# Performance work log

Measured on AMD Instinct MI355X. Metric: run time of the kernel, lower is better.

The kernel has to match this reference:

```python
import jax, jax.numpy as jnp
import numpy as np
import math

R0, R1 = 0.5, 40.0            # radius_range
SP0, SP1 = 8, 8               # social_pooling_size
HID = 48                      # hidden_size
INP = 96                      # input_size (32 img feat + 16 vel + 48 fsp)
N_OTHERS = 400000
RADIUS_STEP = (R1 - R0) / SP0
THETA_STEP = 2.0 * math.pi / SP1


def setup_inputs() -> dict:
    key = jax.random.key(0)
    ks = jax.random.split(key, 20)
    loc_agent = jnp.array([40.0, 10.0], dtype=jnp.float32)  # keeps int image indexing in-range
    loc_others = loc_agent + jax.random.uniform(ks[0], (N_OTHERS, 2), minval=-50.0, maxval=50.0, dtype=jnp.float32)
    loc_other_index = jnp.arange(N_OTHERS, dtype=jnp.int32)
    feature_img = jax.random.normal(ks[1], (1, 32, 80, 80), dtype=jnp.float32)
    f_vel = jax.random.normal(ks[2], (16,), dtype=jnp.float32)
    hiddens = jax.random.normal(ks[3], (N_OTHERS, HID), dtype=jnp.float32)
    hidden = jax.random.normal(ks[4], (HID,), dtype=jnp.float32)
    fan_in = SP0 * SP1 * HID
    lim = 1.0 / np.sqrt(fan_in)
    W_fc = jax.random.uniform(ks[5], (HID, fan_in), minval=-lim, maxval=lim, dtype=jnp.float32)
    b_fc = jax.random.uniform(ks[6], (HID,), minval=-lim, maxval=lim, dtype=jnp.float32)
    weight_ir = jax.random.normal(ks[7], (INP,), dtype=jnp.float32)
    weight_hr = jax.random.normal(ks[8], (HID,), dtype=jnp.float32)
    bias_ir = jax.random.normal(ks[9], (1,), dtype=jnp.float32)
    bias_hr = jax.random.normal(ks[10], (1,), dtype=jnp.float32)
    weight_iz = jax.random.normal(ks[11], (INP,), dtype=jnp.float32)
    weight_hz = jax.random.normal(ks[12], (HID,), dtype=jnp.float32)
    bias_iz = jax.random.normal(ks[13], (1,), dtype=jnp.float32)
    bias_hz = jax.random.normal(ks[14], (1,), dtype=jnp.float32)
    weight_in = jax.random.normal(ks[15], (INP,), dtype=jnp.float32)
    weight_hn = jax.random.normal(ks[16], (HID,), dtype=jnp.float32)
    bias_in = jax.random.normal(ks[17], (1,), dtype=jnp.float32)
    bias_hn = jax.random.normal(ks[18], (1,), dtype=jnp.float32)
    return dict(loc_agent=loc_agent, loc_others=loc_others, loc_other_index=loc_other_index,
                feature_img=feature_img, f_vel=f_vel, hiddens=hiddens, hidden=hidden,
                W_fc=W_fc, b_fc=b_fc,
                weight_ir=weight_ir, weight_hr=weight_hr, bias_ir=bias_ir, bias_hr=bias_hr,
                weight_iz=weight_iz, weight_hz=weight_hz, bias_iz=bias_iz, bias_hz=bias_hz,
                weight_in=weight_in, weight_hn=weight_hn, bias_in=bias_in, bias_hn=bias_hn)


def reference(loc_agent, loc_others, loc_other_index, feature_img, f_vel, hiddens, hidden,
              W_fc, b_fc, weight_ir, weight_hr, bias_ir, bias_hr,
              weight_iz, weight_hz, bias_iz, bias_hz, weight_in, weight_hn, bias_in, bias_hn):
    H = feature_img.shape[2]
    # feature_agent = feature_img[0, :, H/2 - int(y), int(x)]   (truncating int cast, positives)
    u0 = (H // 2) - loc_agent[1].astype(jnp.int32)
    v0 = loc_agent[0].astype(jnp.int32)
    feature_agent = feature_img[0, :, u0, v0]                     # (32,)

    # --- vectorized distance/angle binned scatter-mean social pooling ---
    c = loc_others - loc_agent[None, :]                           # (n,2)
    dist = jnp.sqrt(jnp.sum(c * c, axis=1))                       # (n,)
    safe_dist = jnp.where(dist > 0, dist, 1.0)
    acos = jnp.arccos(jnp.clip(c[:, 0] / safe_dist, -1.0, 1.0))
    theta = jnp.where(c[:, 1] < 0, 2.0 * jnp.pi - acos, acos)     # [0, 2pi)
    mask = (dist >= R0) & (dist <= R1)
    u = jnp.clip(jnp.floor((dist - R0) / RADIUS_STEP), 0, SP0 - 1).astype(jnp.int32)
    v = jnp.clip(jnp.floor(theta / THETA_STEP), 0, SP1 - 1).astype(jnp.int32)
    nbins = SP0 * SP1
    bins = jnp.where(mask, u * SP1 + v, nbins)                    # out-of-range -> dump bin
    gathered = hiddens[loc_other_index]                           # (n,48)
    sp_sum = jax.ops.segment_sum(gathered, bins, num_segments=nbins + 1)[:-1]      # (64,48)
    cnt = jax.ops.segment_sum(mask.astype(hiddens.dtype), bins, num_segments=nbins + 1)[:-1]  # (64,)
    # original divides only when count > 1 (count==1 is a no-op, count==0 stays 0)
    sp = jnp.where(cnt[:, None] > 1.0, sp_sum / jnp.maximum(cnt[:, None], 1.0), sp_sum)
    sp = sp.reshape(nbins * HID)                                  # (3072,)

    fsp = jax.nn.relu(W_fc @ sp + b_fc)                           # (48,)
    input_x = jnp.concatenate([feature_agent, f_vel, fsp], axis=0)  # (96,)

    # scalar-gate GRU (note: rt is computed but unused in the original, ht ignores it)
    rt = jax.nn.sigmoid(jnp.dot(input_x, weight_ir) + bias_ir[0] + jnp.dot(hidden, weight_hr) + bias_hr[0])
    zt = jax.nn.sigmoid(jnp.dot(input_x, weight_iz) + bias_iz[0] + jnp.dot(hidden, weight_hz) + bias_hz[0])
    nt = jnp.tanh(jnp.dot(input_x, weight_in) + bias_in[0] + jnp.dot(hidden, weight_hn) + bias_hn[0])
    ht = (1.0 - zt) * nt + zt * hidden                            # (48,)
    return ht
```

## Files before the change

### kernel.cpp

```cpp
#include <hip/hip_runtime.h>
#include <hip/hip_bf16.h>
#include <math.h>


#define NBINS 64
#define HID 48
#define PAD 49

__global__ void zero_ws_kernel(float* ws) {
    int i = blockIdx.x * blockDim.x + threadIdx.x;
    if (i < NBINS * HID + NBINS) ws[i] = 0.0f;
}

__global__ __launch_bounds__(1024) void bin_accum_kernel(
    const float2* __restrict__ loc_others,
    const float*  __restrict__ loc_agent,
    const int*    __restrict__ loc_other_index,
    const float*  __restrict__ hiddens,
    float* __restrict__ ws_sums,
    float* __restrict__ ws_cnts,
    int n)
{
    __shared__ float s_sum[NBINS * PAD];
    __shared__ float s_cnt[NBINS];
    for (int k = threadIdx.x; k < NBINS * PAD; k += blockDim.x) s_sum[k] = 0.0f;
    if (threadIdx.x < NBINS) s_cnt[threadIdx.x] = 0.0f;
    __syncthreads();

    const float ax = loc_agent[0];
    const float ay = loc_agent[1];

    int t = blockIdx.x * blockDim.x + threadIdx.x;
    int stride = gridDim.x * blockDim.x;
    for (int i = t; i < n; i += stride) {
        float2 p = loc_others[i];
        float cx = p.x - ax;
        float cy = p.y - ay;
        float d = sqrtf(cx * cx + cy * cy);
        if (d < 0.5f || d > 40.0f) continue;

        float ac = acosf(fminf(fmaxf(cx / d, -1.0f), 1.0f));
        float theta = (cy < 0.0f) ? (6.283185307179586f - ac) : ac;

        float uf = floorf((d - 0.5f) / 4.9375f);
        float vf = floorf(theta / 0.7853981633974483f);
        int u = (int)fminf(fmaxf(uf, 0.0f), 7.0f);
        int v = (int)fminf(fmaxf(vf, 0.0f), 7.0f);
        int bin = u * 8 + v;

        int row = loc_other_index[i];
        const float4* hp = (const float4*)(hiddens + (size_t)row * HID);
        float* dst = s_sum + bin * PAD;
        unsafeAtomicAdd(&s_cnt[bin], 1.0f);
#pragma unroll
        for (int k = 0; k < HID / 4; ++k) {
            float4 h = hp[k];
            unsafeAtomicAdd(dst + 4 * k + 0, h.x);
            unsafeAtomicAdd(dst + 4 * k + 1, h.y);
            unsafeAtomicAdd(dst + 4 * k + 2, h.z);
            unsafeAtomicAdd(dst + 4 * k + 3, h.w);
        }
    }
    __syncthreads();

    for (int k = threadIdx.x; k < NBINS * HID; k += blockDim.x) {
        int b = k / HID;
        int j = k - b * HID;
        unsafeAtomicAdd(&ws_sums[k], s_sum[b * PAD + j]);
    }
    if (threadIdx.x < NBINS) unsafeAtomicAdd(&ws_cnts[threadIdx.x], s_cnt[threadIdx.x]);
}

__global__ __launch_bounds__(256) void fc_kernel(
    const float* __restrict__ W_fc,
    const float* __restrict__ b_fc,
    const float* __restrict__ sums,
    const float* __restrict__ cnts,
    float* __restrict__ fsp)
{
    int r = blockIdx.x;
    const float* w = W_fc + (size_t)r * (NBINS * HID);
    float partial = 0.0f;
    for (int k = threadIdx.x; k < NBINS * HID; k += 256) {
        int b = k / HID;
        float c = cnts[b];
        float s = sums[k];
        float sp = (c > 1.0f) ? (s / c) : s;
        partial += w[k] * sp;
    }
    for (int off = 32; off >= 1; off >>= 1) partial += __shfl_down(partial, off, 64);
    __shared__ float red[4];
    if ((threadIdx.x & 63) == 0) red[threadIdx.x >> 6] = partial;
    __syncthreads();
    if (threadIdx.x == 0) {
        float s = red[0] + red[1] + red[2] + red[3];
        fsp[r] = fmaxf(s + b_fc[r], 0.0f);
    }
}

__global__ void gru_kernel(
    const float* __restrict__ feature_img,
    const float* __restrict__ loc_agent,
    const float* __restrict__ f_vel,
    const float* __restrict__ fsp,
    const float* __restrict__ hidden,
    const float* __restrict__ w_iz, const float* __restrict__ w_hz,
    const float* __restrict__ b_iz, const float* __restrict__ b_hz,
    const float* __restrict__ w_in, const float* __restrict__ w_hn,
    const float* __restrict__ b_in, const float* __restrict__ b_hn,
    float* __restrict__ out)
{
    int l = threadIdx.x;
    int u0 = 40 - (int)loc_agent[1];
    int v0 = (int)loc_agent[0];
    int pix = u0 * 80 + v0;

    float pz = 0.0f, pn = 0.0f;
    for (int e = l; e < 96; e += 64) {
        float x;
        if (e < 32)      x = feature_img[e * 6400 + pix];
        else if (e < 48) x = f_vel[e - 32];
        else             x = fsp[e - 48];
        pz += x * w_iz[e];
        pn += x * w_in[e];
    }
    if (l < HID) {
        float h = hidden[l];
        pz += h * w_hz[l];
        pn += h * w_hn[l];
    }
    for (int off = 32; off >= 1; off >>= 1) {
        pz += __shfl_xor(pz, off, 64);
        pn += __shfl_xor(pn, off, 64);
    }
    float zt = 1.0f / (1.0f + expf(-(pz + b_iz[0] + b_hz[0])));
    float nt = tanhf(pn + b_in[0] + b_hn[0]);
    if (l < HID) out[l] = (1.0f - zt) * nt + zt * hidden[l];
}

extern "C" void kernel_launch(void* const* d_in, const int* in_sizes, int n_in,
                              void* d_out, int out_size, void* d_ws, size_t ws_size,
                              hipStream_t stream) {
    const float* loc_agent       = (const float*)d_in[0];
    const float* loc_others      = (const float*)d_in[1];
    const int*   loc_other_index = (const int*)d_in[2];
    const float* feature_img     = (const float*)d_in[3];
    const float* f_vel           = (const float*)d_in[4];
    const float* hiddens         = (const float*)d_in[5];
    const float* hidden          = (const float*)d_in[6];
    const float* W_fc            = (const float*)d_in[7];
    const float* b_fc            = (const float*)d_in[8];
    const float* w_iz            = (const float*)d_in[13];
    const float* w_hz            = (const float*)d_in[14];
    const float* b_iz            = (const float*)d_in[15];
    const float* b_hz            = (const float*)d_in[16];
    const float* w_in            = (const float*)d_in[17];
    const float* w_hn            = (const float*)d_in[18];
    const float* b_in            = (const float*)d_in[19];
    const float* b_hn            = (const float*)d_in[20];

    float* ws   = (float*)d_ws;
    float* sums = ws;
    float* cnts = ws + 3072;
    float* fsp  = ws + 3136;
    float* out  = (float*)d_out;

    int n = in_sizes[2];

    hipLaunchKernelGGL(zero_ws_kernel, dim3(13), dim3(256), 0, stream, ws);
    hipLaunchKernelGGL(bin_accum_kernel, dim3(256), dim3(1024), 0, stream,
                       (const float2*)loc_others, loc_agent, loc_other_index,
                       hiddens, sums, cnts, n);
    hipLaunchKernelGGL(fc_kernel, dim3(48), dim3(256), 0, stream,
                       W_fc, b_fc, sums, cnts, fsp);
    hipLaunchKernelGGL(gru_kernel, dim3(1), dim3(64), 0, stream,
                       feature_img, loc_agent, f_vel, fsp, hidden,
                       w_iz, w_hz, b_iz, b_hz, w_in, w_hn, b_in, b_hn, out);
}
```

Measured before the change: 89.40 us.

## Replace global atomic reduction with per-block partial buffers and combine kernel

Each block now writes its shared-memory bin sums and counts to its own slot in workspace instead of atomically adding into one global accumulator. A new combine kernel sums the partial slots to produce the final sums and counts. When the workspace is too small, blocks share slots and fall back to atomics, with a zeroing pass. This removes contention from 256 blocks atomically adding into the same 3136 floats, at the cost of an extra kernel launch and more workspace traffic.

New measurement: 145.3 us. 1.63x slower.

```diff
diff --git a/kernel.cpp b/kernel.cpp
--- a/kernel.cpp
+++ b/kernel.cpp
@@ -6,10 +6,14 @@
 #define NBINS 64
 #define HID 48
 #define PAD 49
-
-__global__ void zero_ws_kernel(float* ws) {
+#define ENT 3136
+#define SLOT 3200
+#define PART_OFF 3200
+#define FSP_OFF 3136
+
+__global__ void zero_partials_kernel(float* part, int total) {
     int i = blockIdx.x * blockDim.x + threadIdx.x;
-    if (i < NBINS * HID + NBINS) ws[i] = 0.0f;
+    if (i < total) part[i] = 0.0f;
 }
 
 __global__ __launch_bounds__(1024) void bin_accum_kernel(
@@ -17,9 +21,8 @@
     const float*  __restrict__ loc_agent,
     const int*    __restrict__ loc_other_index,
     const float*  __restrict__ hiddens,
-    float* __restrict__ ws_sums,
-    float* __restrict__ ws_cnts,
-    int n)
+    float* __restrict__ part,
+    int n, int P, int direct)
 {
     __shared__ float s_sum[NBINS * PAD];
     __shared__ float s_cnt[NBINS];
@@ -63,12 +66,34 @@
     }
     __syncthreads();
 
-    for (int k = threadIdx.x; k < NBINS * HID; k += blockDim.x) {
-        int b = k / HID;
-        int j = k - b * HID;
-        unsafeAtomicAdd(&ws_sums[k], s_sum[b * PAD + j]);
-    }
-    if (threadIdx.x < NBINS) unsafeAtomicAdd(&ws_cnts[threadIdx.x], s_cnt[threadIdx.x]);
+    float* dst = part + (size_t)(blockIdx.x % P) * SLOT;
+    if (direct) {
+        for (int k = threadIdx.x; k < NBINS * HID; k += blockDim.x) {
+            int b = k / HID;
+            int j = k - b * HID;
+            dst[k] = s_sum[b * PAD + j];
+        }
+        if (threadIdx.x < NBINS) dst[NBINS * HID + threadIdx.x] = s_cnt[threadIdx.x];
+    } else {
+        for (int k = threadIdx.x; k < NBINS * HID; k += blockDim.x) {
+            int b = k / HID;
+            int j = k - b * HID;
+            unsafeAtomicAdd(&dst[k], s_sum[b * PAD + j]);
+        }
+        if (threadIdx.x < NBINS) unsafeAtomicAdd(&dst[NBINS * HID + threadIdx.x], s_cnt[threadIdx.x]);
+    }
+}
+
+__global__ __launch_bounds__(256) void combine_kernel(
+    float* __restrict__ ws,
+    const float* __restrict__ part,
+    int P)
+{
+    int k = blockIdx.x * 256 + threadIdx.x;
+    if (k >= ENT) return;
+    float s = 0.0f;
+    for (int b = 0; b < P; ++b) s += part[(size_t)b * SLOT + k];
+    ws[k] = s;
 }
 
 __global__ __launch_bounds__(256) void fc_kernel(
@@ -161,16 +186,29 @@
 
     float* ws   = (float*)d_ws;
     float* sums = ws;
-    float* cnts = ws + 3072;
-    float* fsp  = ws + 3136;
+    float* cnts = ws + NBINS * HID;
+    float* fsp  = ws + FSP_OFF;
+    float* part = ws + PART_OFF;
     float* out  = (float*)d_out;
 
     int n = in_sizes[2];
 
-    hipLaunchKernelGGL(zero_ws_kernel, dim3(13), dim3(256), 0, stream, ws);
-    hipLaunchKernelGGL(bin_accum_kernel, dim3(256), dim3(1024), 0, stream,
+    const int NBLK = 256;
+    long wfloats = (long)(ws_size / 4);
+    long avail = (wfloats - PART_OFF) / SLOT;
+    int P = (int)(avail < 1 ? 1 : (avail > NBLK ? NBLK : avail));
+    int direct = (P == NBLK) ? 1 : 0;
+
+    if (!direct) {
+        int total = P * SLOT;
+        hipLaunchKernelGGL(zero_partials_kernel, dim3((total + 1023) / 1024),
+                           dim3(1024), 0, stream, part, total);
+    }
+    hipLaunchKernelGGL(bin_accum_kernel, dim3(NBLK), dim3(1024), 0, stream,
                        (const float2*)loc_others, loc_agent, loc_other_index,
-                       hiddens, sums, cnts, n);
+                       hiddens, part, n, P, direct);
+    hipLaunchKernelGGL(combine_kernel, dim3((ENT + 255) / 256), dim3(256), 0, stream,
+                       ws, part, P);
     hipLaunchKernelGGL(fc_kernel, dim3(48), dim3(256), 0, stream,
                        W_fc, b_fc, sums, cnts, fsp);
     hipLaunchKernelGGL(gru_kernel, dim3(1), dim3(64), 0, stream,
```
